# Performance work log

Hardware: AMD Instinct MI355X
Metric: run time of the kernel (lower is better)

The kernel has to match this reference:

```python
import jax, jax.numpy as jnp
import numpy as np

N_NODES = 20000
N_EDGES = 320000
IN_DIM = 128
HID = 64
LATENT = 32
NUM_GRAPHS = 64
NEG_SLOPE = 0.2
BN_EPS = 1e-5


def setup_inputs() -> dict:
    key = jax.random.key(0)
    ks = jax.random.split(key, 24)
    def glorot(k, shape):
        fan_in, fan_out = shape[0], shape[-1]
        lim = (6.0 / (fan_in + fan_out)) ** 0.5
        return jax.random.uniform(k, shape, jnp.float32, -lim, lim)
    inp = {
        "x": jax.random.normal(ks[0], (N_NODES, IN_DIM), jnp.float32),
        "edge_index": jax.random.randint(ks[1], (2, N_EDGES), 0, N_NODES, jnp.int64),
        "batch": jnp.sort(jax.random.randint(ks[2], (N_NODES,), 0, NUM_GRAPHS, jnp.int64)),
        # layer 0: in=128 -> out=64, heads=4
        "Wl0": glorot(ks[3], (IN_DIM, 4 * HID)),
        "Wr0": glorot(ks[4], (IN_DIM, 4 * HID)),
        "att0": glorot(ks[5], (4, HID)),
        "b0": jnp.zeros((4 * HID,), jnp.float32),
        # layer 1: in=256 -> out=64, heads=4
        "Wl1": glorot(ks[6], (4 * HID, 4 * HID)),
        "Wr1": glorot(ks[7], (4 * HID, 4 * HID)),
        "att1": glorot(ks[8], (4, HID)),
        "b1": jnp.zeros((4 * HID,), jnp.float32),
        # layer 2: in=256 -> out=64, heads=1
        "Wl2": glorot(ks[9], (4 * HID, HID)),
        "Wr2": glorot(ks[10], (4 * HID, HID)),
        "att2": glorot(ks[11], (1, HID)),
        "b2": jnp.zeros((HID,), jnp.float32),
        # BatchNorm1d(hidden_dim) in eval mode (running stats)
        "bn_gamma": jax.random.uniform(ks[12], (HID,), jnp.float32, 0.5, 1.5),
        "bn_beta": jax.random.normal(ks[13], (HID,), jnp.float32) * 0.1,
        "bn_mean": jax.random.normal(ks[14], (HID,), jnp.float32) * 0.1,
        "bn_var": jax.random.uniform(ks[15], (HID,), jnp.float32, 0.5, 1.5),
        # fc: hidden -> latent
        "fc_w": glorot(ks[16], (HID, LATENT)),
        "fc_b": jnp.zeros((LATENT,), jnp.float32),
    }
    return inp


def gatv2_layer(h, src, dst, Wl, Wr, att, bias):
    # PyG GATv2Conv (concat=True, negative_slope=0.2, self loops already in src/dst)
    N = h.shape[0]
    H, C = att.shape
    xl = (h @ Wl).reshape(N, H, C)  # source transform
    xr = (h @ Wr).reshape(N, H, C)  # target transform
    e = jax.nn.leaky_relu(xl[src] + xr[dst], NEG_SLOPE)   # [E,H,C]
    logits = jnp.einsum("ehc,hc->eh", e, att)             # [E,H]
    # softmax over incoming edges per destination node
    m = jax.ops.segment_max(logits, dst, num_segments=N)  # [N,H]
    ex = jnp.exp(logits - m[dst])
    denom = jax.ops.segment_sum(ex, dst, num_segments=N)
    alpha = ex / denom[dst]                               # [E,H]
    out = jax.ops.segment_sum(alpha[:, :, None] * xl[src], dst, num_segments=N)
    return out.reshape(N, H * C) + bias


def reference(x, edge_index, batch, Wl0, Wr0, att0, b0, Wl1, Wr1, att1, b1,
              Wl2, Wr2, att2, b2, bn_gamma, bn_beta, bn_mean, bn_var, fc_w, fc_b):
    N = x.shape[0]
    loop = jnp.arange(N, dtype=edge_index.dtype)
    src = jnp.concatenate([edge_index[0], loop])  # add self loops (PyG default)
    dst = jnp.concatenate([edge_index[1], loop])
    h = gatv2_layer(x, src, dst, Wl0, Wr0, att0, b0)   # dropout: eval mode -> identity
    h = gatv2_layer(h, src, dst, Wl1, Wr1, att1, b1)
    h = gatv2_layer(h, src, dst, Wl2, Wr2, att2, b2)   # [N, HID]
    pooled = jax.ops.segment_sum(h, batch, num_segments=NUM_GRAPHS)  # global_add_pool
    bn = (pooled - bn_mean) * jax.lax.rsqrt(bn_var + BN_EPS) * bn_gamma + bn_beta
    return bn @ fc_w + fc_b  # [NUM_GRAPHS, LATENT]
```

## Files before the change

### kernel.cpp

```cpp
#include <hip/hip_runtime.h>
#include <math.h>

#define N_NODES 20000
#define E_ORIG  320000
#define NUM_GRAPHS 64
#define SLOTS 64
#define FILLB 1250

typedef __attribute__((ext_vector_type(8))) short bf16x8;
typedef __attribute__((ext_vector_type(4))) float f32x4;

__device__ __forceinline__ ushort f2bf(float x) {
  unsigned u = __float_as_uint(x);
  return (ushort)((u + 0x7fffu + ((u >> 16) & 1u)) >> 16);
}
__device__ __forceinline__ float4 ld_bf16x4(const ushort* p) {
  ushort4 u = *(const ushort4*)p;
  float4 f;
  f.x = __uint_as_float((unsigned)u.x << 16);
  f.y = __uint_as_float((unsigned)u.y << 16);
  f.z = __uint_as_float((unsigned)u.z << 16);
  f.w = __uint_as_float((unsigned)u.w << 16);
  return f;
}
__device__ __forceinline__ void gl_lds16(const void* g, void* l) {
  __builtin_amdgcn_global_load_lds(
      (const __attribute__((address_space(1))) unsigned*)(uintptr_t)g,
      (__attribute__((address_space(3))) unsigned*)(uintptr_t)l, 16, 0, 0);
}

__global__ __launch_bounds__(256) void prep(
    const float* __restrict__ x,
    const float* __restrict__ Wl0, const float* __restrict__ Wr0,
    const float* __restrict__ Wl1, const float* __restrict__ Wr1,
    const float* __restrict__ Wl2, const float* __restrict__ Wr2,
    ushort* __restrict__ x16, ushort* __restrict__ Bt0,
    ushort* __restrict__ Bt1, ushort* __restrict__ Bt2,
    int* __restrict__ cursor)
{
  const int Z0 = 640000;
  const int Z1 = Z0 + 65536;
  const int Z2 = Z1 + 131072;
  const int Z3 = Z2 + 32768;
  const int Z4 = Z3 + N_NODES / 4;
  int t = blockIdx.x * 256 + threadIdx.x;
  if (t < Z0) {
    int i = t << 2;
    float4 v = *(const float4*)&x[i];
    ushort4 o; o.x = f2bf(v.x); o.y = f2bf(v.y); o.z = f2bf(v.z); o.w = f2bf(v.w);
    *(ushort4*)&x16[i] = o;
  } else if (t < Z1) {
    int idx = t - Z0; int n = idx >> 7, k = idx & 127;
    float v = (n < 256) ? Wl0[k * 256 + n] : Wr0[k * 256 + (n - 256)];
    Bt0[idx] = f2bf(v);
  } else if (t < Z2) {
    int idx = t - Z1; int n = idx >> 8, k = idx & 255;
    float v = (n < 256) ? Wl1[k * 256 + n] : Wr1[k * 256 + (n - 256)];
    Bt1[idx] = f2bf(v);
  } else if (t < Z3) {
    int idx = t - Z2; int n = idx >> 8, k = idx & 255;
    float v = (n < 64) ? Wl2[k * 64 + n] : Wr2[k * 64 + (n - 64)];
    Bt2[idx] = f2bf(v);
  } else if (t < Z4) {
    int4 z = {0, 0, 0, 0};
    *(int4*)&cursor[(t - Z3) << 2] = z;
  }
}

__device__ __forceinline__ void gemm_body(
    const ushort* __restrict__ A, const ushort* __restrict__ Bt,
    ushort* __restrict__ XL, ushort* __restrict__ XR,
    int M, int K, int N, int bid, int tid, char* smem)
{
  ushort* As = (ushort*)smem;
  ushort* Bs = As + 8192;

  const int mtiles = (M + 127) >> 7;
  const int xcd = bid & 7;
  const int i = bid >> 3;
  const int n0 = (i / 20) << 7;
  const int m = xcd + ((i % 20) << 3);
  if (m >= mtiles) return;
  const int m0 = m << 7;

  const int lane = tid & 63;
  const int w = tid >> 6;
  const int wm = (w >> 1) << 6;
  const int wn = (w & 1) << 6;
  const int quad = lane >> 4;
  const int l15 = lane & 15;

  f32x4 acc[4][4] = {};

  for (int k0 = 0; k0 < K; k0 += 64) {
    #pragma unroll
    for (int r = 0; r < 4; r++) {
      int c = (r << 8) + tid;
      int row = c >> 3;
      int col = (c & 7) << 3;
      int ga = m0 + row; if (ga >= M) ga = M - 1;
      gl_lds16(A  + (size_t)ga * K + k0 + col, (char*)As + c * 16);
      gl_lds16(Bt + (size_t)(n0 + row) * K + k0 + col, (char*)Bs + c * 16);
    }
    __syncthreads();
    #pragma unroll
    for (int ks = 0; ks < 2; ks++) {
      bf16x8 af[4], bfr[4];
      #pragma unroll
      for (int ii = 0; ii < 4; ii++)
        af[ii]  = *(const bf16x8*)&As[(wm + (ii << 4) + l15) * 64 + (ks << 5) + (quad << 3)];
      #pragma unroll
      for (int j = 0; j < 4; j++)
        bfr[j] = *(const bf16x8*)&Bs[(wn + (j << 4) + l15) * 64 + (ks << 5) + (quad << 3)];
      #pragma unroll
      for (int ii = 0; ii < 4; ii++)
        #pragma unroll
        for (int j = 0; j < 4; j++)
          acc[ii][j] = __builtin_amdgcn_mfma_f32_16x16x32_bf16(
              af[ii], bfr[j], acc[ii][j], 0, 0, 0);
    }
    __syncthreads();
  }

  ushort* Cs = (ushort*)smem + w * 4608;
  #pragma unroll
  for (int ii = 0; ii < 4; ii++)
    #pragma unroll
    for (int j = 0; j < 4; j++)
      #pragma unroll
      for (int r = 0; r < 4; r++)
        Cs[((ii << 4) + (quad << 2) + r) * 72 + (j << 4) + l15] = f2bf(acc[ii][j][r]);
  const int Nh = N >> 1;
  const int colbase = n0 + wn;
  ushort* Cc = (colbase < Nh) ? (XL + colbase) : (XR + (colbase - Nh));
  #pragma unroll
  for (int it = 0; it < 8; it++) {
    int row = (it << 3) + (lane >> 3);
    int cc = lane & 7;
    bf16x8 v = *(const bf16x8*)&Cs[row * 72 + (cc << 3)];
    int grow = m0 + wm + row;
    if (grow < M)
      *(bf16x8*)&Cc[(size_t)grow * Nh + (cc << 3)] = v;
  }
}

__global__ __launch_bounds__(256) void mfma_gemm_bf16(
    const ushort* __restrict__ A, const ushort* __restrict__ Bt,
    ushort* __restrict__ XL, ushort* __restrict__ XR, int M, int K, int N)
{
  __shared__ char smem[36864];
  gemm_body(A, Bt, XL, XR, M, K, N, blockIdx.x, threadIdx.x, smem);
}

__global__ __launch_bounds__(256) void gemm0_fill(
    const ushort* __restrict__ x16, const ushort* __restrict__ Bt0,
    ushort* __restrict__ XL, ushort* __restrict__ XR,
    const int* __restrict__ esrc, const int* __restrict__ edst,
    int* __restrict__ cursor, int* __restrict__ csr_src)
{
  __shared__ char smem[36864];
  const int bid = blockIdx.x;
  if (bid < FILLB) {
    int e = bid * 256 + threadIdx.x;
    if (e >= E_ORIG) return;
    int src = esrc[e], dst = edst[e];
    int pos = atomicAdd(&cursor[dst], 1);
    if (pos < SLOTS) csr_src[((size_t)dst << 6) + pos] = src;
    return;
  }
  gemm_body(x16, Bt0, XL, XR, N_NODES, 128, 512, bid - FILLB, threadIdx.x, smem);
}

__device__ __forceinline__ void h4_edge(
    const float4& xv, const float4& xrv, const float4& attv,
    float4& acc, float& lsum)
{
  float4 a;
  a.x = xv.x + xrv.x; a.y = xv.y + xrv.y;
  a.z = xv.z + xrv.z; a.w = xv.w + xrv.w;
  a.x = fmaxf(a.x, 0.2f * a.x); a.y = fmaxf(a.y, 0.2f * a.y);
  a.z = fmaxf(a.z, 0.2f * a.z); a.w = fmaxf(a.w, 0.2f * a.w);
  float v = a.x * attv.x + a.y * attv.y + a.z * attv.z + a.w * attv.w;
  v += __shfl_xor(v, 1);
  v += __shfl_xor(v, 2);
  v += __shfl_xor(v, 4);
  v += __shfl_xor(v, 8);
  float w = __expf(v);
  lsum += w;
  acc.x += w * xv.x; acc.y += w * xv.y;
  acc.z += w * xv.z; acc.w += w * xv.w;
}

__global__ __launch_bounds__(256) void gat_gather_h4(
    const ushort* __restrict__ XL, const ushort* __restrict__ XR,
    const float* __restrict__ att, const float* __restrict__ bias,
    const int* __restrict__ cnt, const int* __restrict__ csr,
    ushort* __restrict__ hout)
{
  const int n = blockIdx.x * 4 + (threadIdx.x >> 6);
  const int lane = threadIdx.x & 63;
  const int c4 = lane << 2;
  const float4 xrv  = ld_bf16x4(XR + (size_t)n * 256 + c4);
  const float4 attv = *(const float4*)&att[c4];
  float4 acc = make_float4(0.f, 0.f, 0.f, 0.f);
  float lsum = 0.f;
  {
    float4 xs = ld_bf16x4(XL + (size_t)n * 256 + c4);
    h4_edge(xs, xrv, attv, acc, lsum);
  }
  const int beg = n << 6;
  int deg = cnt[n]; if (deg > SLOTS) deg = SLOTS;
  const int end = beg + deg;
  int p = beg;
  for (; p + 7 < end; p += 8) {
    int s0 = csr[p],     s1 = csr[p + 1];
    int s2 = csr[p + 2], s3 = csr[p + 3];
    int s4 = csr[p + 4], s5 = csr[p + 5];
    int s6 = csr[p + 6], s7 = csr[p + 7];
    float4 x0 = ld_bf16x4(XL + (size_t)s0 * 256 + c4);
    float4 x1 = ld_bf16x4(XL + (size_t)s1 * 256 + c4);
    float4 x2 = ld_bf16x4(XL + (size_t)s2 * 256 + c4);
    float4 x3 = ld_bf16x4(XL + (size_t)s3 * 256 + c4);
    float4 x4 = ld_bf16x4(XL + (size_t)s4 * 256 + c4);
    float4 x5 = ld_bf16x4(XL + (size_t)s5 * 256 + c4);
    float4 x6 = ld_bf16x4(XL + (size_t)s6 * 256 + c4);
    float4 x7 = ld_bf16x4(XL + (size_t)s7 * 256 + c4);
    h4_edge(x0, xrv, attv, acc, lsum);
    h4_edge(x1, xrv, attv, acc, lsum);
    h4_edge(x2, xrv, attv, acc, lsum);
    h4_edge(x3, xrv, attv, acc, lsum);
    h4_edge(x4, xrv, attv, acc, lsum);
    h4_edge(x5, xrv, attv, acc, lsum);
    h4_edge(x6, xrv, attv, acc, lsum);
    h4_edge(x7, xrv, attv, acc, lsum);
  }
  for (; p + 3 < end; p += 4) {
    int s0 = csr[p],     s1 = csr[p + 1];
    int s2 = csr[p + 2], s3 = csr[p + 3];
    float4 x0 = ld_bf16x4(XL + (size_t)s0 * 256 + c4);
    float4 x1 = ld_bf16x4(XL + (size_t)s1 * 256 + c4);
    float4 x2 = ld_bf16x4(XL + (size_t)s2 * 256 + c4);
    float4 x3 = ld_bf16x4(XL + (size_t)s3 * 256 + c4);
    h4_edge(x0, xrv, attv, acc, lsum);
    h4_edge(x1, xrv, attv, acc, lsum);
    h4_edge(x2, xrv, attv, acc, lsum);
    h4_edge(x3, xrv, attv, acc, lsum);
  }
  for (; p < end; p++) {
    int s0 = csr[p];
    float4 x0 = ld_bf16x4(XL + (size_t)s0 * 256 + c4);
    h4_edge(x0, xrv, attv, acc, lsum);
  }
  const float4 bv = *(const float4*)&bias[c4];
  float inv = 1.f / lsum;
  ushort4 o;
  o.x = f2bf(acc.x * inv + bv.x); o.y = f2bf(acc.y * inv + bv.y);
  o.z = f2bf(acc.z * inv + bv.z); o.w = f2bf(acc.w * inv + bv.w);
  *(ushort4*)&hout[(size_t)n * 256 + c4] = o;
}

__global__ __launch_bounds__(256) void gat_gather_h1(
    const ushort* __restrict__ XL, const ushort* __restrict__ XR,
    const float* __restrict__ att, const float* __restrict__ bias,
    const int* __restrict__ cnt, const int* __restrict__ csr,
    float* __restrict__ h3)
{
  const int n = blockIdx.x * 4 + (threadIdx.x >> 6);
  const int lane = threadIdx.x & 63;
  const int g = lane >> 4, c4 = (lane & 15) << 2;
  const float4 xrv  = ld_bf16x4(XR + (size_t)n * 64 + c4);
  const float4 attv = *(const float4*)&att[c4];
  float4 acc = make_float4(0.f, 0.f, 0.f, 0.f);
  float lsum = 0.f;
  if (g == 0) {
    float4 xs = ld_bf16x4(XL + (size_t)n * 64 + c4);
    h4_edge(xs, xrv, attv, acc, lsum);
  }
  const int beg = n << 6;
  int deg = cnt[n]; if (deg > SLOTS) deg = SLOTS;
  const int end = beg + deg;
  int p = beg + g;
  for (; p + 4 < end; p += 8) {
    int s0 = csr[p], s1 = csr[p + 4];
    float4 x0 = ld_bf16x4(XL + (size_t)s0 * 64 + c4);
    float4 x1 = ld_bf16x4(XL + (size_t)s1 * 64 + c4);
    h4_edge(x0, xrv, attv, acc, lsum);
    h4_edge(x1, xrv, attv, acc, lsum);
  }
  if (p < end) {
    int s0 = csr[p];
    float4 x0 = ld_bf16x4(XL + (size_t)s0 * 64 + c4);
    h4_edge(x0, xrv, attv, acc, lsum);
  }
  #pragma unroll
  for (int off = 16; off <= 32; off <<= 1) {
    lsum  += __shfl_xor(lsum, off);
    acc.x += __shfl_xor(acc.x, off); acc.y += __shfl_xor(acc.y, off);
    acc.z += __shfl_xor(acc.z, off); acc.w += __shfl_xor(acc.w, off);
  }
  if (g == 0) {
    const float4 bv = *(const float4*)&bias[c4];
    float inv = 1.f / lsum;
    float4 o;
    o.x = acc.x * inv + bv.x; o.y = acc.y * inv + bv.y;
    o.z = acc.z * inv + bv.z; o.w = acc.w * inv + bv.w;
    *(float4*)&h3[(size_t)n * 64 + c4] = o;
  }
}

__global__ __launch_bounds__(256) void pool_bn_fc(
    const float* __restrict__ h3, const int* __restrict__ batch,
    const float* __restrict__ gamma, const float* __restrict__ beta,
    const float* __restrict__ mean, const float* __restrict__ var,
    const float* __restrict__ fcw, const float* __restrict__ fcb,
    float* __restrict__ out)
{
  __shared__ float red[256];
  __shared__ float s[64];
  const int g = blockIdx.x;
  const int t = threadIdx.x;
  const int c = t & 63, r = t >> 6;
  int lo = 0, hi = N_NODES;
  while (lo < hi) { int mid = (lo + hi) >> 1; if (batch[mid] < g) lo = mid + 1; else hi = mid; }
  int s0 = lo;
  hi = N_NODES;
  while (lo < hi) { int mid = (lo + hi) >> 1; if (batch[mid] < g + 1) lo = mid + 1; else hi = mid; }
  int e0 = lo;
  float a = 0.f;
  for (int n = s0 + r; n < e0; n += 4) a += h3[(size_t)n * 64 + c];
  red[t] = a;
  __syncthreads();
  if (r == 0) {
    float p = red[c] + red[c + 64] + red[c + 128] + red[c + 192];
    s[c] = (p - mean[c]) * rsqrtf(var[c] + 1e-5f) * gamma[c] + beta[c];
  }
  __syncthreads();
  if (t < 32) {
    float acc = fcb[t];
    #pragma unroll
    for (int k = 0; k < 64; k++) acc += s[k] * fcw[k * 32 + t];
    out[g * 32 + t] = acc;
  }
}

extern "C" void kernel_launch(void* const* d_in, const int* in_sizes, int n_in,
                              void* d_out, int out_size, void* d_ws, size_t ws_size,
                              hipStream_t stream) {
  const float* x    = (const float*)d_in[0];
  const int*   ei   = (const int*)d_in[1];
  const int*   batch= (const int*)d_in[2];
  const float* Wl0  = (const float*)d_in[3];
  const float* Wr0  = (const float*)d_in[4];
  const float* att0 = (const float*)d_in[5];
  const float* b0   = (const float*)d_in[6];
  const float* Wl1  = (const float*)d_in[7];
  const float* Wr1  = (const float*)d_in[8];
  const float* att1 = (const float*)d_in[9];
  const float* b1   = (const float*)d_in[10];
  const float* Wl2  = (const float*)d_in[11];
  const float* Wr2  = (const float*)d_in[12];
  const float* att2 = (const float*)d_in[13];
  const float* b2   = (const float*)d_in[14];
  const float* bng  = (const float*)d_in[15];
  const float* bnb  = (const float*)d_in[16];
  const float* bnm  = (const float*)d_in[17];
  const float* bnv  = (const float*)d_in[18];
  const float* fcw  = (const float*)d_in[19];
  const float* fcb  = (const float*)d_in[20];
  float* out = (float*)d_out;

  const int* esrc = ei;
  const int* edst = ei + E_ORIG;

  char* w = (char*)d_ws;
  ushort* x16  = (ushort*)w;                 w += (size_t)N_NODES * 128 * 2;
  ushort* XL   = (ushort*)w;                 w += (size_t)N_NODES * 256 * 2;
  ushort* XR   = (ushort*)w;                 w += (size_t)N_NODES * 256 * 2;
  ushort* h16  = (ushort*)w;                 w += (size_t)N_NODES * 256 * 2;
  ushort* XL2  = (ushort*)w;                 w += (size_t)N_NODES * 64 * 2;
  ushort* XR2  = (ushort*)w;                 w += (size_t)N_NODES * 64 * 2;
  float*  h3   = (float*)w;                  w += (size_t)N_NODES * 64 * 4;
  ushort* Bt0  = (ushort*)w;                 w += (size_t)512 * 128 * 2;
  ushort* Bt1  = (ushort*)w;                 w += (size_t)512 * 256 * 2;
  ushort* Bt2  = (ushort*)w;                 w += (size_t)128 * 256 * 2;
  int* cursor  = (int*)w;                    w += (size_t)N_NODES * 4;
  int* csr     = (int*)w;

  dim3 blk(256);

  prep<<<dim3(3416), blk, 0, stream>>>(
      x, Wl0, Wr0, Wl1, Wr1, Wl2, Wr2, x16, Bt0, Bt1, Bt2, cursor);

  gemm0_fill<<<dim3(FILLB + 160 * 4), blk, 0, stream>>>(
      x16, Bt0, XL, XR, esrc, edst, cursor, csr);

  gat_gather_h4<<<dim3(N_NODES / 4), blk, 0, stream>>>(
      XL, XR, att0, b0, cursor, csr, h16);

  mfma_gemm_bf16<<<dim3(160 * 4), blk, 0, stream>>>(h16, Bt1, XL, XR, N_NODES, 256, 512);
  gat_gather_h4<<<dim3(N_NODES / 4), blk, 0, stream>>>(
      XL, XR, att1, b1, cursor, csr, h16);

  mfma_gemm_bf16<<<dim3(160 * 1), blk, 0, stream>>>(h16, Bt2, XL2, XR2, N_NODES, 256, 128);
  gat_gather_h1<<<dim3(N_NODES / 4), blk, 0, stream>>>(
      XL2, XR2, att2, b2, cursor, csr, h3);

  pool_bn_fc<<<dim3(NUM_GRAPHS), blk, 0, stream>>>(
      h3, batch, bng, bnb, bnm, bnv, fcw, fcb, out);
}
```

Before: 262.4 us.

## Store GEMM outputs head-major and split H4 gather per head with XCD mapping

The GEMM epilogue now writes XL/XR in a head-major layout ([head][node][64]), so each head's features form a contiguous 2.5MB slab. The 4-head gather kernel launches one block per (head, node group) and maps block IDs so each head lands on a fixed pair of XCDs. That should keep each head's slab resident in that XCD's L2. Each wave splits edges across 4 lane groups, each handling 16 channels, and combines the partial sums with shuffles. The aim is better L2 locality for the random-source gathers, at the cost of 4x more blocks, extra shuffle reductions, and a strided 128B write pattern to hout.

```diff
diff --git a/kernel.cpp b/kernel.cpp
--- a/kernel.cpp
+++ b/kernel.cpp
@@ -132,7 +132,8 @@
         Cs[((ii << 4) + (quad << 2) + r) * 72 + (j << 4) + l15] = f2bf(acc[ii][j][r]);
   const int Nh = N >> 1;
   const int colbase = n0 + wn;
-  ushort* Cc = (colbase < Nh) ? (XL + colbase) : (XR + (colbase - Nh));
+  const int cb = (colbase < Nh) ? colbase : (colbase - Nh);
+  ushort* Cc = ((colbase < Nh) ? XL : XR) + (size_t)(cb >> 6) * M * 64;
   #pragma unroll
   for (int it = 0; it < 8; it++) {
     int row = (it << 3) + (lane >> 3);
@@ -140,7 +141,7 @@
     bf16x8 v = *(const bf16x8*)&Cs[row * 72 + (cc << 3)];
     int grow = m0 + wm + row;
     if (grow < M)
-      *(bf16x8*)&Cc[(size_t)grow * Nh + (cc << 3)] = v;
+      *(bf16x8*)&Cc[(size_t)grow * 64 + (cc << 3)] = v;
   }
 }
 
@@ -192,71 +193,71 @@
 }
 
 __global__ __launch_bounds__(256) void gat_gather_h4(
-    const ushort* __restrict__ XL, const ushort* __restrict__ XR,
+    const ushort* __restrict__ XLh, const ushort* __restrict__ XRh,
     const float* __restrict__ att, const float* __restrict__ bias,
     const int* __restrict__ cnt, const int* __restrict__ csr,
     ushort* __restrict__ hout)
 {
-  const int n = blockIdx.x * 4 + (threadIdx.x >> 6);
+  const int bid = blockIdx.x;
+  const int xcd = bid & 7;
+  const int h = xcd >> 1;
+  const int sub = ((bid >> 3) << 1) | (xcd & 1);
+  const int wv = threadIdx.x >> 6;
+  const int n = sub * 4 + wv;
   const int lane = threadIdx.x & 63;
-  const int c4 = lane << 2;
-  const float4 xrv  = ld_bf16x4(XR + (size_t)n * 256 + c4);
-  const float4 attv = *(const float4*)&att[c4];
+  const int g = lane >> 4, c4 = (lane & 15) << 2;
+  const ushort* XL = XLh + (size_t)h * N_NODES * 64;
+  const ushort* XR = XRh + (size_t)h * N_NODES * 64;
+  const float4 xrv  = ld_bf16x4(XR + (size_t)n * 64 + c4);
+  const float4 attv = *(const float4*)&att[h * 64 + c4];
   float4 acc = make_float4(0.f, 0.f, 0.f, 0.f);
   float lsum = 0.f;
-  {
-    float4 xs = ld_bf16x4(XL + (size_t)n * 256 + c4);
+  if (g == 0) {
+    float4 xs = ld_bf16x4(XL + (size_t)n * 64 + c4);
     h4_edge(xs, xrv, attv, acc, lsum);
   }
   const int beg = n << 6;
   int deg = cnt[n]; if (deg > SLOTS) deg = SLOTS;
   const int end = beg + deg;
-  int p = beg;
-  for (; p + 7 < end; p += 8) {
-    int s0 = csr[p],     s1 = csr[p + 1];
-    int s2 = csr[p + 2], s3 = csr[p + 3];
-    int s4 = csr[p + 4], s5 = csr[p + 5];
-    int s6 = csr[p + 6], s7 = csr[p + 7];
-    float4 x0 = ld_bf16x4(XL + (size_t)s0 * 256 + c4);
-    float4 x1 = ld_bf16x4(XL + (size_t)s1 * 256 + c4);
-    float4 x2 = ld_bf16x4(XL + (size_t)s2 * 256 + c4);
-    float4 x3 = ld_bf16x4(XL + (size_t)s3 * 256 + c4);
-    float4 x4 = ld_bf16x4(XL + (size_t)s4 * 256 + c4);
-    float4 x5 = ld_bf16x4(XL + (size_t)s5 * 256 + c4);
-    float4 x6 = ld_bf16x4(XL + (size_t)s6 * 256 + c4);
-    float4 x7 = ld_bf16x4(XL + (size_t)s7 * 256 + c4);
+  int p = beg + g;
+  for (; p + 12 < end; p += 16) {
+    int s0 = csr[p],     s1 = csr[p + 4];
+    int s2 = csr[p + 8], s3 = csr[p + 12];
+    float4 x0 = ld_bf16x4(XL + (size_t)s0 * 64 + c4);
+    float4 x1 = ld_bf16x4(XL + (size_t)s1 * 64 + c4);
+    float4 x2 = ld_bf16x4(XL + (size_t)s2 * 64 + c4);
+    float4 x3 = ld_bf16x4(XL + (size_t)s3 * 64 + c4);
     h4_edge(x0, xrv, attv, acc, lsum);
     h4_edge(x1, xrv, attv, acc, lsum);
     h4_edge(x2, xrv, attv, acc, lsum);
     h4_edge(x3, xrv, attv, acc, lsum);
-    h4_edge(x4, xrv, attv, acc, lsum);
-    h4_edge(x5, xrv, attv, acc, lsum);
-    h4_edge(x6, xrv, attv, acc, lsum);
-    h4_edge(x7, xrv, attv, acc, lsum);
-  }
-  for (; p + 3 < end; p += 4) {
-    int s0 = csr[p],     s1 = csr[p + 1];
-    int s2 = csr[p + 2], s3 = csr[p + 3];
-    float4 x0 = ld_bf16x4(XL + (size_t)s0 * 256 + c4);
-    float4 x1 = ld_bf16x4(XL + (size_t)s1 * 256 + c4);
-    float4 x2 = ld_bf16x4(XL + (size_t)s2 * 256 + c4);
-    float4 x3 = ld_bf16x4(XL + (size_t)s3 * 256 + c4);
+  }
+  for (; p + 4 < end; p += 8) {
+    int s0 = csr[p], s1 = csr[p + 4];
+    float4 x0 = ld_bf16x4(XL + (size_t)s0 * 64 + c4);
+    float4 x1 = ld_bf16x4(XL + (size_t)s1 * 64 + c4);
     h4_edge(x0, xrv, attv, acc, lsum);
     h4_edge(x1, xrv, attv, acc, lsum);
-    h4_edge(x2, xrv, attv, acc, lsum);
-    h4_edge(x3, xrv, attv, acc, lsum);
-  }
-  for (; p < end; p++) {
+  }
+  if (p < end) {
     int s0 = csr[p];
-    float4 x0 = ld_bf16x4(XL + (size_t)s0 * 256 + c4);
+    float4 x0 = ld_bf16x4(XL + (size_t)s0 * 64 + c4);
     h4_edge(x0, xrv, attv, acc, lsum);
   }
-  const float4 bv = *(const float4*)&bias[c4];
-  float inv = 1.f / lsum;
-  ushort4 o;
-  o.x = f2bf(acc.x * inv + bv.x); o.y = f2bf(acc.y * inv + bv.y);
-  o.z = f2bf(acc.z * inv + bv.z); o.w = f2bf(acc.w * inv + bv.w);
-  *(ushort4*)&hout[(size_t)n * 256 + c4] = o;
+  #pragma unroll
+  for (int off = 16; off <= 32; off <<= 1) {
+    lsum  += __shfl_xor(lsum, off);
+    acc.x += __shfl_xor(acc.x, off); acc.y += __shfl_xor(acc.y, off);
+    acc.z += __shfl_xor(acc.z, off); acc.w += __shfl_xor(acc.w, off);
+  }
+  if (g == 0) {
+    const float4 bv = *(const float4*)&bias[h * 64 + c4];
+    float inv = 1.f / lsum;
+    ushort4 o;
+    o.x = f2bf(acc.x * inv + bv.x); o.y = f2bf(acc.y * inv + bv.y);
+    o.z = f2bf(acc.z * inv + bv.z); o.w = f2bf(acc.w * inv + bv.w);
+    *(ushort4*)&hout[(size_t)n * 256 + h * 64 + c4] = o;
+  }
 }
 
 __global__ __launch_bounds__(256) void gat_gather_h1(
@@ -394,11 +395,11 @@
   gemm0_fill<<<dim3(FILLB + 160 * 4), blk, 0, stream>>>(
       x16, Bt0, XL, XR, esrc, edst, cursor, csr);
 
-  gat_gather_h4<<<dim3(N_NODES / 4), blk, 0, stream>>>(
+  gat_gather_h4<<<dim3(N_NODES), blk, 0, stream>>>(
       XL, XR, att0, b0, cursor, csr, h16);
 
   mfma_gemm_bf16<<<dim3(160 * 4), blk, 0, stream>>>(h16, Bt1, XL, XR, N_NODES, 256, 512);
-  gat_gather_h4<<<dim3(N_NODES / 4), blk, 0, stream>>>(
+  gat_gather_h4<<<dim3(N_NODES), blk, 0, stream>>>(
       XL, XR, att1, b1, cursor, csr, h16);
 
   mfma_gemm_bf16<<<dim3(160 * 1), blk, 0, stream>>>(h16, Bt2, XL2, XR2, N_NODES, 256, 128);
```

Measured after the change: 303.2 us. 1.16x slower.
